# Optimization experiments

Hardware: AMD Instinct MI355X
Metric: run time of the kernel (lower is better)

The kernel has to match this reference:

```python
import jax, jax.numpy as jnp
import numpy as np

N, E, F, H, L = 10000, 200000, 28, 256, 6
NUM_ATOM, NUM_BOND = 100, 24

def ssp(x):
    # shifted softplus used by SchNet
    return jax.nn.softplus(x) - jnp.log(2.0)

def setup_inputs() -> dict:
    key = jax.random.key(0)
    ks = iter(jax.random.split(key, 64))
    def nrm(shape, scale=0.05):
        return jax.random.normal(next(ks), shape, dtype=jnp.float32) * scale
    inp = {}
    inp['atom_type'] = jax.random.randint(next(ks), (N,), 0, NUM_ATOM)
    inp['r_feat'] = jax.random.normal(next(ks), (N, F), dtype=jnp.float32)
    inp['p_feat'] = jax.random.normal(next(ks), (N, F), dtype=jnp.float32)
    inp['pos'] = jax.random.normal(next(ks), (N, 3), dtype=jnp.float32) * 3.0
    inp['edge_index'] = jax.random.randint(next(ks), (2, E), 0, N)
    inp['edge_type_r'] = jax.random.randint(next(ks), (E,), 0, NUM_BOND)
    inp['edge_type_p'] = jax.random.randint(next(ks), (E,), 0, NUM_BOND)
    # learned parameters
    inp['atom_emb_table'] = nrm((NUM_ATOM, H // 2), 1.0)
    inp['feat_W'] = nrm((F, H // 2))                       # atom_feat_embedding (no bias)
    inp['bond_emb_table'] = nrm((NUM_BOND, H), 1.0)        # edge encoder bond embedding
    inp['edge_mlp_W1'] = nrm((1, H)); inp['edge_mlp_b1'] = jnp.zeros((H,), jnp.float32)
    inp['edge_mlp_W2'] = nrm((H, H)); inp['edge_mlp_b2'] = jnp.zeros((H,), jnp.float32)
    inp['cat_W1'] = nrm((2 * H, H)); inp['cat_b1'] = jnp.zeros((H,), jnp.float32)
    inp['cat_W2'] = nrm((H, H)); inp['cat_b2'] = jnp.zeros((H,), jnp.float32)
    # SchNet interaction blocks, stacked over L layers
    inp['filt_W1'] = nrm((L, H, H)); inp['filt_b1'] = jnp.zeros((L, H), jnp.float32)
    inp['filt_W2'] = nrm((L, H, H)); inp['filt_b2'] = jnp.zeros((L, H), jnp.float32)
    inp['lin1_W'] = nrm((L, H, H))
    inp['lin2_W'] = nrm((L, H, H)); inp['lin2_b'] = jnp.zeros((L, H), jnp.float32)
    inp['lin3_W'] = nrm((L, H, H)); inp['lin3_b'] = jnp.zeros((L, H), jnp.float32)
    # grad_global_dist_mlp: 2H -> H -> H/2 -> 1
    inp['grad_W1'] = nrm((2 * H, H)); inp['grad_b1'] = jnp.zeros((H,), jnp.float32)
    inp['grad_W2'] = nrm((H, H // 2)); inp['grad_b2'] = jnp.zeros((H // 2,), jnp.float32)
    inp['grad_W3'] = nrm((H // 2, 1)); inp['grad_b3'] = jnp.zeros((1,), jnp.float32)
    return inp

def _forward(r_feat, p_feat, pos, atom_emb_table, feat_W, bond_emb_table,
             edge_mlp_W1, edge_mlp_b1, edge_mlp_W2, edge_mlp_b2,
             cat_W1, cat_b1, cat_W2, cat_b2,
             filt_W1, filt_b1, filt_W2, filt_b2,
             lin1_W, lin2_W, lin2_b, lin3_W, lin3_b,
             grad_W1, grad_b1, grad_W2, grad_b2, grad_W3, grad_b3,
             atom_type, edge_index, edge_type_r, edge_type_p):
    src, dst = edge_index[0], edge_index[1]
    # node embedding: z = [atom_emb + feat(r), feat(p) - feat(r)]
    ar = r_feat @ feat_W
    ap = p_feat @ feat_W
    z = jnp.concatenate([atom_emb_table[atom_type] + ar, ap - ar], axis=-1)  # (N, H)
    # edge lengths (E, 1)
    d = pos[src] - pos[dst]
    edge_length = jnp.sqrt(jnp.sum(d * d, axis=-1, keepdims=True) + 1e-12)
    # condensed edge embedding 'bond_w_d': mlp(d) * bond_emb(type), r/p branches, then edge_cat MLP
    d_emb = ssp(edge_length @ edge_mlp_W1 + edge_mlp_b1) @ edge_mlp_W2 + edge_mlp_b2  # (E, H)
    attr_r = d_emb * bond_emb_table[edge_type_r]
    attr_p = d_emb * bond_emb_table[edge_type_p]
    edge_attr = jax.nn.relu(jnp.concatenate([attr_r, attr_p], -1) @ cat_W1 + cat_b1) @ cat_W2 + cat_b2  # (E, H)
    # SchNet encoder: L CFConv interaction blocks with residual
    nn_ = z.shape[0]
    def layer(h, p):
        fW1, fb1, fW2, fb2, l1, l2, l2b, l3, l3b = p
        Wf = ssp(edge_attr @ fW1 + fb1) @ fW2 + fb2            # (E, H) continuous filters
        msg = (h @ l1)[src] * Wf                               # gather + modulate
        agg = jax.ops.segment_sum(msg, dst, num_segments=nn_)  # scatter-add to nodes
        return h + (ssp(agg @ l2 + l2b) @ l3 + l3b), None
    node_attr, _ = jax.lax.scan(layer, z, (filt_W1, filt_b1, filt_W2, filt_b2, lin1_W, lin2_W, lin2_b, lin3_W, lin3_b))
    # assemble_atom_pair_feature: [h_row * h_col, edge_attr] -> (E, 2H)
    h_pair = jnp.concatenate([node_attr[src] * node_attr[dst], edge_attr], axis=-1)
    h = jax.nn.relu(h_pair @ grad_W1 + grad_b1)
    h = jax.nn.relu(h @ grad_W2 + grad_b2)
    edge_inv = h @ grad_W3 + grad_b3                           # (E, 1)
    return edge_inv, edge_length

def reference(atom_type, r_feat, p_feat, pos, edge_index, edge_type_r, edge_type_p,
              atom_emb_table, feat_W, bond_emb_table,
              edge_mlp_W1, edge_mlp_b1, edge_mlp_W2, edge_mlp_b2,
              cat_W1, cat_b1, cat_W2, cat_b2,
              filt_W1, filt_b1, filt_W2, filt_b2,
              lin1_W, lin2_W, lin2_b, lin3_W, lin3_b,
              grad_W1, grad_b1, grad_W2, grad_b2, grad_W3, grad_b3):
    return _forward(r_feat, p_feat, pos, atom_emb_table, feat_W, bond_emb_table,
                    edge_mlp_W1, edge_mlp_b1, edge_mlp_W2, edge_mlp_b2,
                    cat_W1, cat_b1, cat_W2, cat_b2,
                    filt_W1, filt_b1, filt_W2, filt_b2,
                    lin1_W, lin2_W, lin2_b, lin3_W, lin3_b,
                    grad_W1, grad_b1, grad_W2, grad_b2, grad_W3, grad_b3,
                    atom_type, edge_index, edge_type_r, edge_type_p)
```

## Files before the change

### kernel.cpp

```cpp
#include <hip/hip_runtime.h>
#include <hip/hip_bf16.h>
#include <math.h>

#define HDIM 256

typedef unsigned short u16;
typedef short short8 __attribute__((ext_vector_type(8)));
typedef _Float16 f16x8 __attribute__((ext_vector_type(8)));
typedef float f32x4 __attribute__((ext_vector_type(4)));

__device__ __forceinline__ float sspf(float x) {
  const float LOG2E = 1.4426950408889634f, LN2 = 0.6931471805599453f;
  float t = exp2f(-fabsf(x) * LOG2E);
  return fmaxf(x, 0.f) + (log2f(1.f + t) - 1.f) * LN2;
}
__device__ __forceinline__ float bf2f(u16 u) {
  union { unsigned int i; float f; } x; x.i = ((unsigned int)u) << 16; return x.f;
}
__device__ __forceinline__ u16 f2bf(float f) {
  union { float f; unsigned int i; } x; x.f = f;
  unsigned int r = x.i + 0x7FFFu + ((x.i >> 16) & 1u);
  return (u16)(r >> 16);
}
__device__ __forceinline__ u16 f2h_bits(float f) {
  _Float16 h = (_Float16)f;
  return __builtin_bit_cast(unsigned short, h);
}
__device__ __forceinline__ float4 ld4f(const float* p) { return *(const float4*)p; }

__device__ __forceinline__ int iw_idx(int row, int col) {
  return row * 256 + ((((col >> 3) ^ (row & 7)) << 3) | (col & 7));
}
__device__ __forceinline__ int ir_idx(int row, int cchunk) {
  return row * 256 + ((cchunk ^ (row & 7)) << 3);
}

template<int DT>
__device__ __forceinline__ f32x4 mma(short8 a, short8 b, f32x4 c) {
  if constexpr (DT == 0)
    return __builtin_amdgcn_mfma_f32_16x16x32_bf16(a, b, c, 0, 0, 0);
  else
    return __builtin_amdgcn_mfma_f32_16x16x32_f16(__builtin_bit_cast(f16x8, a),
                                                  __builtin_bit_cast(f16x8, b), c, 0, 0, 0);
}

__device__ __forceinline__ void zacc(f32x4 (&acc)[4][4]) {
#pragma unroll
  for (int i = 0; i < 4; ++i)
#pragma unroll
    for (int j = 0; j < 4; ++j) { acc[i][j][0]=0.f; acc[i][j][1]=0.f; acc[i][j][2]=0.f; acc[i][j][3]=0.f; }
}

template<int NSTEPS, int BT_N, int NTW, int DT, bool WRAP8, typename ATR>
__device__ __forceinline__ void gemm44(f32x4 (&acc)[4][4], const u16* __restrict__ bt,
                                       const u16* __restrict__ inter,
                                       int w, int m, int quad, ATR atr) {
#pragma unroll
  for (int ks = 0; ks < NSTEPS; ++ks) {
    short8 bf[NTW];
#pragma unroll
    for (int nt = 0; nt < NTW; ++nt)
      bf[nt] = *(const short8*)(bt + (size_t)ks * (BT_N * 32)
                                + (w * (NTW * 16) + nt * 16 + m) * 32 + quad * 8);
    int kchunk = (WRAP8 ? (ks & 7) : ks) * 4 + quad;
#pragma unroll
    for (int mt = 0; mt < 4; ++mt) {
      short8 af = *(const short8*)&inter[ir_idx(mt * 16 + m, kchunk)];
      af = atr(mt, ks, af);
#pragma unroll
      for (int nt = 0; nt < NTW; ++nt)
        acc[mt][nt] = mma<DT>(af, bf[nt], acc[mt][nt]);
    }
  }
}

template<int NTW, int ACT, int OF>
__device__ __forceinline__ void store_inter44(u16* inter, int w, int m, int quad,
                                              const f32x4 (&acc)[4][4], const float* bias) {
#pragma unroll
  for (int mt = 0; mt < 4; ++mt)
#pragma unroll
    for (int nt = 0; nt < NTW; ++nt) {
      int col = w * (NTW * 16) + nt * 16 + m;
      float bv = bias[col];
#pragma unroll
      for (int r = 0; r < 4; ++r) {
        int row = mt * 16 + quad * 4 + r;
        float x = acc[mt][nt][r] + bv;
        if (ACT == 1) x = fmaxf(x, 0.f);
        else if (ACT == 2) x = sspf(x);
        inter[iw_idx(row, col)] = (OF == 0) ? f2bf(x) : f2h_bits(x);
      }
    }
}

template<int NTW, int ACT>
__device__ __forceinline__ void store_edge44(u16* C, int row0, int w, int m, int quad,
                                             const f32x4 (&acc)[4][4], const float* bias) {
#pragma unroll
  for (int mt = 0; mt < 4; ++mt)
#pragma unroll
    for (int nt = 0; nt < NTW; ++nt) {
      int col = w * (NTW * 16) + nt * 16 + m;
      float bv = bias[col];
#pragma unroll
      for (int r = 0; r < 4; ++r) {
        float x = acc[mt][nt][r] + bv;
        if (ACT == 1) x = fmaxf(x, 0.f);
        C[(size_t)(row0 + mt * 16 + quad * 4 + r) * HDIM + col] = f2bf(x);
      }
    }
}

template<int NTW, int ACT, int CM>
__device__ __forceinline__ void store_node44(float* C, int row0, int w, int m, int quad,
                                             const f32x4 (&acc)[4][4], const float* bias, int M) {
#pragma unroll
  for (int mt = 0; mt < 4; ++mt)
#pragma unroll
    for (int nt = 0; nt < NTW; ++nt) {
      int col = w * (NTW * 16) + nt * 16 + m;
      float bv = bias ? bias[col] : 0.f;
#pragma unroll
      for (int r = 0; r < 4; ++r) {
        int row = row0 + mt * 16 + quad * 4 + r;
        if (row < M) {
          float x = acc[mt][nt][r] + bv;
          if (ACT == 2) x = sspf(x);
          size_t idx = (size_t)row * HDIM + col;
          if (CM == 1) x += C[idx];
          C[idx] = x;
        }
      }
    }
}

struct EncArgs {
  const int* se_e; const float* lenp; const float* W1; const float* b1;
  const u16* btA; const float* bA;
  const float* bondT; const int* etr; const int* etp;
  const u16* btB; const float* bB;
  const u16* btC; const float* bC;
  u16* outp;
};
__global__ __launch_bounds__(256, 3) void encoder_k(EncArgs a) {
  __shared__ u16 inter[64 * 256];
  __shared__ u16 bondL[24 * 264];
  const int t = threadIdx.x;
  const int w = t >> 6, lane = t & 63, m = lane & 15, quad = lane >> 4;
  const int row0 = blockIdx.x * 64;
  auto idt = [](int, int, short8 v) { return v; };

  for (int i = t; i < 24 * 256; i += 256) {
    int r = i >> 8, c = i & 255;
    bondL[r * 264 + c] = f2h_bits(a.bondT[r * 256 + c]);
  }
  int brv[4], bpv[4];
#pragma unroll
  for (int mt = 0; mt < 4; ++mt) {
    int eo = a.se_e[row0 + mt * 16 + m];
    brv[mt] = a.etr[eo]; bpv[mt] = a.etp[eo];
  }
  {
    int row = t >> 2;
    float len = a.lenp[a.se_e[row0 + row]];
#pragma unroll
    for (int c = 0; c < 8; ++c) {
      int chunk = (t & 3) + c * 4, k = chunk * 8;
      float4 w0 = ld4f(a.W1 + k), w1 = ld4f(a.W1 + k + 4);
      float4 c0 = ld4f(a.b1 + k), c1 = ld4f(a.b1 + k + 4);
      short8 v;
      v[0] = (short)f2bf(sspf(len * w0.x + c0.x)); v[1] = (short)f2bf(sspf(len * w0.y + c0.y));
      v[2] = (short)f2bf(sspf(len * w0.z + c0.z)); v[3] = (short)f2bf(sspf(len * w0.w + c0.w));
      v[4] = (short)f2bf(sspf(len * w1.x + c1.x)); v[5] = (short)f2bf(sspf(len * w1.y + c1.y));
      v[6] = (short)f2bf(sspf(len * w1.z + c1.z)); v[7] = (short)f2bf(sspf(len * w1.w + c1.w));
      *(short8*)&inter[row * 256 + ((chunk ^ (row & 7)) << 3)] = v;
    }
  }
  __syncthreads();
  f32x4 acc[4][4];
  zacc(acc);
  gemm44<8, 256, 4, 0, false>(acc, a.btA, inter, w, m, quad, idt);
  __syncthreads();
  store_inter44<4, 0, 1>(inter, w, m, quad, acc, a.bA);
  __syncthreads();
  zacc(acc);
  auto atrB = [&](int mt, int ks, short8 v) -> short8 {
    int k2 = (ks & 7) * 32 + quad * 8;
    int et = (ks < 8) ? brv[mt] : bpv[mt];
    f16x8 dv = __builtin_bit_cast(f16x8, v);
    f16x8 bd = __builtin_bit_cast(f16x8, *(const short8*)&bondL[et * 264 + k2]);
    return __builtin_bit_cast(short8, dv * bd);
  };
  gemm44<16, 256, 4, 1, true>(acc, a.btB, inter, w, m, quad, atrB);
  __syncthreads();
  store_inter44<4, 1, 0>(inter, w, m, quad, acc, a.bB);
  __syncthreads();
  zacc(acc);
  gemm44<8, 256, 4, 0, false>(acc, a.btC, inter, w, m, quad, idt);
  store_edge44<4, 0>(a.outp, row0, w, m, quad, acc, a.bC);
}

struct FiltArgs { const u16* inA; const u16* bt1; const float* b1; const u16* bt2; const float* b2; u16* outp; };
__global__ __launch_bounds__(256, 3) void filt_k(FiltArgs a) {
  __shared__ u16 inter[64 * 256];
  const int t = threadIdx.x;
  const int w = t >> 6, lane = t & 63, m = lane & 15, quad = lane >> 4;
  const int row0 = blockIdx.x * 64;
  auto idt = [](int, int, short8 v) { return v; };
  {
    int row = t >> 2;
#pragma unroll
    for (int c = 0; c < 8; ++c) {
      int chunk = (t & 3) + c * 4;
      short8 v = *(const short8*)(a.inA + (size_t)(row0 + row) * HDIM + chunk * 8);
      *(short8*)&inter[row * 256 + ((chunk ^ (row & 7)) << 3)] = v;
    }
  }
  __syncthreads();
  f32x4 acc[4][4];
  zacc(acc);
  gemm44<8, 256, 4, 0, false>(acc, a.bt1, inter, w, m, quad, idt);
  __syncthreads();
  store_inter44<4, 2, 0>(inter, w, m, quad, acc, a.b1);
  __syncthreads();
  zacc(acc);
  gemm44<8, 256, 4, 0, false>(acc, a.bt2, inter, w, m, quad, idt);
  store_edge44<4, 0>(a.outp, row0, w, m, quad, acc, a.b2);
}

struct GradArgs {
  const float* h; const int* se_src; const int* se_dst; const int* se_e;
  const u16* eA; const u16* bt1; const float* b1; const u16* bt2; const float* b2;
  const float* W3; const float* b3; float* outp;
};
__global__ __launch_bounds__(256, 3) void gradf_k(GradArgs a) {
  __shared__ u16 inter[64 * 256];
  const int t = threadIdx.x;
  const int w = t >> 6, lane = t & 63, m = lane & 15, quad = lane >> 4;
  const int row0 = blockIdx.x * 64;
  auto idt = [](int, int, short8 v) { return v; };
  {
    int row = t >> 2;
    int s = a.se_src[row0 + row], d = a.se_dst[row0 + row];
#pragma unroll
    for (int c = 0; c < 8; ++c) {
      int chunk = (t & 3) + c * 4, k = chunk * 8;
      const float* xp = a.h + (size_t)s * HDIM + k;
      const float* yp = a.h + (size_t)d * HDIM + k;
      float4 x0 = ld4f(xp), x1 = ld4f(xp + 4);
      float4 y0 = ld4f(yp), y1 = ld4f(yp + 4);
      short8 v;
      v[0] = (short)f2bf(x0.x * y0.x); v[1] = (short)f2bf(x0.y * y0.y);
      v[2] = (short)f2bf(x0.z * y0.z); v[3] = (short)f2bf(x0.w * y0.w);
      v[4] = (short)f2bf(x1.x * y1.x); v[5] = (short)f2bf(x1.y * y1.y);
      v[6] = (short)f2bf(x1.z * y1.z); v[7] = (short)f2bf(x1.w * y1.w);
      *(short8*)&inter[row * 256 + ((chunk ^ (row & 7)) << 3)] = v;
    }
  }
  __syncthreads();
  f32x4 acc[4][4];
  zacc(acc);
  gemm44<8, 256, 4, 0, false>(acc, a.bt1, inter, w, m, quad, idt);
  __syncthreads();
  {
    int row = t >> 2;
#pragma unroll
    for (int c = 0; c < 8; ++c) {
      int chunk = (t & 3) + c * 4;
      short8 v = *(const short8*)(a.eA + (size_t)(row0 + row) * HDIM + chunk * 8);
      *(short8*)&inter[row * 256 + ((chunk ^ (row & 7)) << 3)] = v;
    }
  }
  __syncthreads();
  gemm44<8, 256, 4, 0, false>(acc, a.bt1 + 8 * 256 * 32, inter, w, m, quad, idt);
  __syncthreads();
  store_inter44<4, 1, 0>(inter, w, m, quad, acc, a.b1);
  __syncthreads();
  zacc(acc);
  gemm44<8, 128, 2, 0, false>(acc, a.bt2, inter, w, m, quad, idt);
  float p[4][4];
#pragma unroll
  for (int mt = 0; mt < 4; ++mt) { p[mt][0]=0.f; p[mt][1]=0.f; p[mt][2]=0.f; p[mt][3]=0.f; }
#pragma unroll
  for (int mt = 0; mt < 4; ++mt)
#pragma unroll
    for (int nt = 0; nt < 2; ++nt) {
      int col = w * 32 + nt * 16 + m;
      float w3 = a.W3[col], bv = a.b2[col];
#pragma unroll
      for (int r = 0; r < 4; ++r) p[mt][r] += fmaxf(acc[mt][nt][r] + bv, 0.f) * w3;
    }
  __syncthreads();
  float* red = (float*)inter;
#pragma unroll
  for (int mt = 0; mt < 4; ++mt)
#pragma unroll
    for (int r = 0; r < 4; ++r)
      red[(mt * 16 + quad * 4 + r) * 68 + w * 16 + m] = p[mt][r];
  __syncthreads();
  if (t < 64) {
    float s = a.b3[0];
#pragma unroll
    for (int i = 0; i < 64; ++i) s += red[t * 68 + i];
    a.outp[a.se_e[row0 + t]] = s;
  }
}

struct LinArgs { const float* A; const u16* bt; float* C; int M; };
__global__ __launch_bounds__(256, 3) void lin1_k(LinArgs a) {
  __shared__ u16 inter[64 * 256];
  const int t = threadIdx.x;
  const int w = t >> 6, lane = t & 63, m = lane & 15, quad = lane >> 4;
  const int row0 = blockIdx.x * 64;
  auto idt = [](int, int, short8 v) { return v; };
  {
    int row = t >> 2, grow = row0 + row;
#pragma unroll
    for (int c = 0; c < 8; ++c) {
      int chunk = (t & 3) + c * 4, k = chunk * 8;
      short8 v;
      if (grow < a.M) {
        const float* p = a.A + (size_t)grow * HDIM + k;
        float4 x0 = ld4f(p), x1 = ld4f(p + 4);
        v[0]=(short)f2bf(x0.x); v[1]=(short)f2bf(x0.y); v[2]=(short)f2bf(x0.z); v[3]=(short)f2bf(x0.w);
        v[4]=(short)f2bf(x1.x); v[5]=(short)f2bf(x1.y); v[6]=(short)f2bf(x1.z); v[7]=(short)f2bf(x1.w);
      } else { v = short8{0,0,0,0,0,0,0,0}; }
      *(short8*)&inter[row * 256 + ((chunk ^ (row & 7)) << 3)] = v;
    }
  }
  __syncthreads();
  f32x4 acc[4][4];
  zacc(acc);
  gemm44<8, 256, 4, 0, false>(acc, a.bt, inter, w, m, quad, idt);
  store_node44<4, 0, 0>(a.C, row0, w, m, quad, acc, nullptr, a.M);
}

struct Lin23Args { const float* A; const u16* bt2; const float* b2; const u16* bt3; const float* b3; float* C; int M; };
__global__ __launch_bounds__(256, 3) void lin23_k(Lin23Args a) {
  __shared__ u16 inter[64 * 256];
  const int t = threadIdx.x;
  const int w = t >> 6, lane = t & 63, m = lane & 15, quad = lane >> 4;
  const int row0 = blockIdx.x * 64;
  auto idt = [](int, int, short8 v) { return v; };
  {
    int row = t >> 2, grow = row0 + row;
#pragma unroll
    for (int c = 0; c < 8; ++c) {
      int chunk = (t & 3) + c * 4, k = chunk * 8;
      short8 v;
      if (grow < a.M) {
        const float* p = a.A + (size_t)grow * HDIM + k;
        float4 x0 = ld4f(p), x1 = ld4f(p + 4);
        v[0]=(short)f2bf(x0.x); v[1]=(short)f2bf(x0.y); v[2]=(short)f2bf(x0.z); v[3]=(short)f2bf(x0.w);
        v[4]=(short)f2bf(x1.x); v[5]=(short)f2bf(x1.y); v[6]=(short)f2bf(x1.z); v[7]=(short)f2bf(x1.w);
      } else { v = short8{0,0,0,0,0,0,0,0}; }
      *(short8*)&inter[row * 256 + ((chunk ^ (row & 7)) << 3)] = v;
    }
  }
  __syncthreads();
  f32x4 acc[4][4];
  zacc(acc);
  gemm44<8, 256, 4, 0, false>(acc, a.bt2, inter, w, m, quad, idt);
  __syncthreads();
  store_inter44<4, 2, 0>(inter, w, m, quad, acc, a.b2);
  __syncthreads();
  zacc(acc);
  gemm44<8, 256, 4, 0, false>(acc, a.bt3, inter, w, m, quad, idt);
  store_node44<4, 0, 1>(a.C, row0, w, m, quad, acc, a.b3, a.M);
}

struct WTDesc { const float* src; u16* dst; int K; int Nshift; int fmt; };
struct WTList { WTDesc d[35]; };
__global__ __launch_bounds__(256) void wtrans_k(WTList wl) {
  WTDesc e = wl.d[blockIdx.y];
  int total = e.K << e.Nshift;
  int idx = blockIdx.x * 256 + threadIdx.x;
  if (idx >= total) return;
  int k = idx >> e.Nshift;
  int n = idx & ((1 << e.Nshift) - 1);
  float v = e.src[idx];
  e.dst[((size_t)(k >> 5) << (e.Nshift + 5)) + n * 32 + (k & 31)] = e.fmt ? f2h_bits(v) : f2bf(v);
}

__global__ void node_embed_k(const int* atom_type, const float* r_feat, const float* p_feat,
                             const float* emb, const float* fW, float* z, int N, int F) {
  int n = blockIdx.x;
  int j = threadIdx.x;
  __shared__ float rr[32], pp[32];
  if (j < F) { rr[j] = r_feat[(size_t)n * F + j]; pp[j] = p_feat[(size_t)n * F + j]; }
  __syncthreads();
  float ar = 0.f, ap = 0.f;
  for (int f = 0; f < F; ++f) {
    float wv = fW[f * 128 + j];
    ar += rr[f] * wv;
    ap += pp[f] * wv;
  }
  int at = atom_type[n];
  z[(size_t)n * HDIM + j] = emb[at * 128 + j] + ar;
  z[(size_t)n * HDIM + 128 + j] = ap - ar;
}

__global__ void edge_geom_k(const float* pos, const int* src, const int* dst, float* len_out, int E) {
  int e = blockIdx.x * blockDim.x + threadIdx.x;
  if (e >= E) return;
  int s = src[e], d = dst[e];
  float dx = pos[s * 3 + 0] - pos[d * 3 + 0];
  float dy = pos[s * 3 + 1] - pos[d * 3 + 1];
  float dz = pos[s * 3 + 2] - pos[d * 3 + 2];
  len_out[e] = sqrtf(dx * dx + dy * dy + dz * dz + 1e-12f);
}

__global__ void zero_k(float4* p, int n4) {
  int i = blockIdx.x * 256 + threadIdx.x;
  if (i < n4) p[i] = make_float4(0.f, 0.f, 0.f, 0.f);
}
__global__ void zero_int_k(int* p, int n) {
  int i = blockIdx.x * 256 + threadIdx.x;
  if (i < n) p[i] = 0;
}
__global__ void hist_k(const int* dst, int* cnt, int E) {
  int e = blockIdx.x * 256 + threadIdx.x;
  if (e < E) atomicAdd(&cnt[dst[e]], 1);
}
__global__ __launch_bounds__(256) void scan_k(const int* cnt, int* rowstart, int N) {
  __shared__ int part[256];
  int t = threadIdx.x;
  int chunk = (N + 255) / 256;
  int lo = t * chunk, hi = lo + chunk; if (hi > N) hi = N; if (lo > N) lo = N;
  int s = 0;
  for (int i = lo; i < hi; ++i) s += cnt[i];
  part[t] = s;
  __syncthreads();
  for (int off = 1; off < 256; off <<= 1) {
    int v = (t >= off) ? part[t - off] : 0;
    __syncthreads();
    part[t] += v;
    __syncthreads();
  }
  int run = (t == 0) ? 0 : part[t - 1];
  for (int i = lo; i < hi; ++i) { rowstart[i] = run; run += cnt[i]; }
  if (t == 255) rowstart[N] = run;
}
__global__ void fill_k(const int* src, const int* dst, const int* rowstart, int* cursor,
                       int* se_src, int* se_dst, int* se_e, int E) {
  int e = blockIdx.x * 256 + threadIdx.x;
  if (e >= E) return;
  int d = dst[e];
  int p = atomicAdd(&cursor[d], 1);
  int idx = rowstart[d] + p;
  se_src[idx] = src[e];
  se_dst[idx] = d;
  se_e[idx] = e;
}

__global__ __launch_bounds__(256) void gather_k(const float* hh, const u16* Wf,
                                                const int* se_src, const int* rowstart,
                                                float* agg, int N) {
  int n = blockIdx.x;
  int j = threadIdx.x;
  int s0 = rowstart[n], s1 = rowstart[n + 1];
  float acc = 0.f;
  for (int i = s0; i < s1; ++i)
    acc += hh[(size_t)se_src[i] * HDIM + j] * bf2f(Wf[(size_t)i * HDIM + j]);
  agg[(size_t)n * HDIM + j] = acc;
}

extern "C" void kernel_launch(void* const* d_in, const int* in_sizes, int n_in,
                              void* d_out, int out_size, void* d_ws, size_t ws_size,
                              hipStream_t stream) {
  const int* atom_type = (const int*)d_in[0];
  const float* r_feat  = (const float*)d_in[1];
  const float* p_feat  = (const float*)d_in[2];
  const float* pos     = (const float*)d_in[3];
  const int* eidx      = (const int*)d_in[4];
  const int* etype_r   = (const int*)d_in[5];
  const int* etype_p   = (const int*)d_in[6];
  const float* atom_emb = (const float*)d_in[7];
  const float* feat_W   = (const float*)d_in[8];
  const float* bondT    = (const float*)d_in[9];
  const float* e_W1     = (const float*)d_in[10];
  const float* e_b1     = (const float*)d_in[11];
  const float* e_W2     = (const float*)d_in[12];
  const float* e_b2     = (const float*)d_in[13];
  const float* cat_W1   = (const float*)d_in[14];
  const float* cat_b1   = (const float*)d_in[15];
  const float* cat_W2   = (const float*)d_in[16];
  const float* cat_b2   = (const float*)d_in[17];
  const float* filt_W1  = (const float*)d_in[18];
  const float* filt_b1  = (const float*)d_in[19];
  const float* filt_W2  = (const float*)d_in[20];
  const float* filt_b2  = (const float*)d_in[21];
  const float* lin1_W   = (const float*)d_in[22];
  const float* lin2_W   = (const float*)d_in[23];
  const float* lin2_b   = (const float*)d_in[24];
  const float* lin3_W   = (const float*)d_in[25];
  const float* lin3_b   = (const float*)d_in[26];
  const float* grad_W1  = (const float*)d_in[27];
  const float* grad_b1  = (const float*)d_in[28];
  const float* grad_W2  = (const float*)d_in[29];
  const float* grad_b2  = (const float*)d_in[30];
  const float* grad_W3  = (const float*)d_in[31];
  const float* grad_b3  = (const float*)d_in[32];

  const int N = in_sizes[0];
  const int F = in_sizes[1] / N;
  const int E = in_sizes[4] / 2;
  const int L = in_sizes[18] / (HDIM * HDIM);
  const int* srcI = eidx;
  const int* dstI = eidx + E;
  float* out = (float*)d_out;

  const size_t BT_ELEMS = (size_t)(32 * 65536 + 2 * 131072 + 32768);
  size_t need = 2 * (size_t)E * HDIM * 2 + 3 * (size_t)N * HDIM * 4 + BT_ELEMS * 2
              + (size_t)(3 * E + 3 * N + 1) * 4 + 64;
  if (ws_size < need) {
    int n4 = (out_size + 3) / 4;
    zero_k<<<(n4 + 255) / 256, 256, 0, stream>>>((float4*)d_out, n4);
    return;
  }
  char* base = (char*)d_ws;
  u16* eA = (u16*)base; base += (size_t)E * HDIM * 2;
  u16* Wf = (u16*)base; base += (size_t)E * HDIM * 2;
  float* h   = (float*)base; base += (size_t)N * HDIM * 4;
  float* hh  = (float*)base; base += (size_t)N * HDIM * 4;
  float* agg = (float*)base; base += (size_t)N * HDIM * 4;
  u16* bt = (u16*)base; base += BT_ELEMS * 2;
  int* se_src = (int*)base; base += (size_t)E * 4;
  int* se_dst = (int*)base; base += (size_t)E * 4;
  int* se_e   = (int*)base; base += (size_t)E * 4;
  int* cnt    = (int*)base; base += (size_t)N * 4;
  int* cursor = (int*)base; base += (size_t)N * 4;
  int* rowstart = (int*)base; base += ((size_t)N + 1) * 4;

  size_t off = 0;
  u16* bt_eW2  = bt + off; off += 65536;
  u16* bt_cat1 = bt + off; off += 131072;
  u16* bt_cat2 = bt + off; off += 65536;
  u16* bt_f1[6]; u16* bt_f2[6]; u16* bt_l1[6]; u16* bt_l2[6]; u16* bt_l3[6];
  for (int l = 0; l < 6; ++l) { bt_f1[l] = bt + off; off += 65536; }
  for (int l = 0; l < 6; ++l) { bt_f2[l] = bt + off; off += 65536; }
  for (int l = 0; l < 6; ++l) { bt_l1[l] = bt + off; off += 65536; }
  for (int l = 0; l < 6; ++l) { bt_l2[l] = bt + off; off += 65536; }
  for (int l = 0; l < 6; ++l) { bt_l3[l] = bt + off; off += 65536; }
  u16* bt_g1 = bt + off; off += 131072;
  u16* bt_g2 = bt + off; off += 32768;

  WTList wl;
  int wi = 0;
  wl.d[wi++] = WTDesc{e_W2, bt_eW2, 256, 8, 0};
  wl.d[wi++] = WTDesc{cat_W1, bt_cat1, 512, 8, 1};
  wl.d[wi++] = WTDesc{cat_W2, bt_cat2, 256, 8, 0};
  for (int l = 0; l < 6; ++l) wl.d[wi++] = WTDesc{filt_W1 + (size_t)l * 65536, bt_f1[l], 256, 8, 0};
  for (int l = 0; l < 6; ++l) wl.d[wi++] = WTDesc{filt_W2 + (size_t)l * 65536, bt_f2[l], 256, 8, 0};
  for (int l = 0; l < 6; ++l) wl.d[wi++] = WTDesc{lin1_W + (size_t)l * 65536, bt_l1[l], 256, 8, 0};
  for (int l = 0; l < 6; ++l) wl.d[wi++] = WTDesc{lin2_W + (size_t)l * 65536, bt_l2[l], 256, 8, 0};
  for (int l = 0; l < 6; ++l) wl.d[wi++] = WTDesc{lin3_W + (size_t)l * 65536, bt_l3[l], 256, 8, 0};
  wl.d[wi++] = WTDesc{grad_W1, bt_g1, 512, 8, 0};
  wl.d[wi++] = WTDesc{grad_W2, bt_g2, 256, 7, 0};
  wtrans_k<<<dim3(512, 35), 256, 0, stream>>>(wl);

  const int EB = E / 64;
  const int NBK = (N + 63) / 64;
  const int EBLK = (E + 255) / 256;

  zero_int_k<<<(2 * N + 255) / 256, 256, 0, stream>>>(cnt, 2 * N);
  hist_k<<<EBLK, 256, 0, stream>>>(dstI, cnt, E);
  scan_k<<<1, 256, 0, stream>>>(cnt, rowstart, N);
  fill_k<<<EBLK, 256, 0, stream>>>(srcI, dstI, rowstart, cursor, se_src, se_dst, se_e, E);

  node_embed_k<<<N, 128, 0, stream>>>(atom_type, r_feat, p_feat, atom_emb, feat_W, h, N, F);
  edge_geom_k<<<EBLK, 256, 0, stream>>>(pos, srcI, dstI, out + E, E);

  EncArgs ea;
  ea.se_e = se_e; ea.lenp = out + E; ea.W1 = e_W1; ea.b1 = e_b1;
  ea.btA = bt_eW2; ea.bA = e_b2;
  ea.bondT = bondT; ea.etr = etype_r; ea.etp = etype_p;
  ea.btB = bt_cat1; ea.bB = cat_b1;
  ea.btC = bt_cat2; ea.bC = cat_b2;
  ea.outp = eA;
  encoder_k<<<EB, 256, 0, stream>>>(ea);

  for (int l = 0; l < L; ++l) {
    const size_t bo = (size_t)l * HDIM;
    FiltArgs fa{eA, bt_f1[l], filt_b1 + bo, bt_f2[l], filt_b2 + bo, Wf};
    filt_k<<<EB, 256, 0, stream>>>(fa);
    LinArgs la{h, bt_l1[l], hh, N};
    lin1_k<<<NBK, 256, 0, stream>>>(la);
    gather_k<<<N, 256, 0, stream>>>(hh, Wf, se_src, rowstart, agg, N);
    Lin23Args l23{agg, bt_l2[l], lin2_b + bo, bt_l3[l], lin3_b + bo, h, N};
    lin23_k<<<NBK, 256, 0, stream>>>(l23);
  }

  GradArgs ga;
  ga.h = h; ga.se_src = se_src; ga.se_dst = se_dst; ga.se_e = se_e;
  ga.eA = eA; ga.bt1 = bt_g1; ga.b1 = grad_b1; ga.bt2 = bt_g2; ga.b2 = grad_b2;
  ga.W3 = grad_W3; ga.b3 = grad_b3; ga.outp = out;
  gradf_k<<<EB, 256, 0, stream>>>(ga);
}
```

Measured before the change: 1.686 ms.

## Fuse filter MLP with neighbor gather via segmented atomic accumulation

Each layer's filter MLP kernel now keeps the bf16 filter output in shared memory and immediately multiplies it by gathered hh[src] rows. It then accumulates runs of equal destination node within the 64-edge tile and flushes each run to agg with float atomics, replacing the separate Wf buffer and per-node gather kernel. This removes a 200000x256 bf16 write and read per layer. It adds a zeroing pass for agg, atomic contention at tile boundaries and nondeterministic summation order. The encoder output store is also staged through padded shared memory for coalesced vector writes.

```diff
diff --git a/kernel.cpp b/kernel.cpp
--- a/kernel.cpp
+++ b/kernel.cpp
@@ -3,6 +3,7 @@
 #include <math.h>
 
 #define HDIM 256
+#define PSTR 264
 
 typedef unsigned short u16;
 typedef short short8 __attribute__((ext_vector_type(8)));
@@ -95,8 +96,8 @@
 }
 
 template<int NTW, int ACT>
-__device__ __forceinline__ void store_edge44(u16* C, int row0, int w, int m, int quad,
-                                             const f32x4 (&acc)[4][4], const float* bias) {
+__device__ __forceinline__ void store_plain44(u16* inter, int w, int m, int quad,
+                                              const f32x4 (&acc)[4][4], const float* bias) {
 #pragma unroll
   for (int mt = 0; mt < 4; ++mt)
 #pragma unroll
@@ -107,9 +108,18 @@
       for (int r = 0; r < 4; ++r) {
         float x = acc[mt][nt][r] + bv;
         if (ACT == 1) x = fmaxf(x, 0.f);
-        C[(size_t)(row0 + mt * 16 + quad * 4 + r) * HDIM + col] = f2bf(x);
+        inter[(mt * 16 + quad * 4 + r) * PSTR + col] = f2bf(x);
       }
     }
+}
+
+__device__ __forceinline__ void copy_out(u16* C, int row0, const u16* inter, int t) {
+#pragma unroll
+  for (int c = 0; c < 8; ++c) {
+    int idx = c * 256 + t;
+    int row = idx >> 5, c8 = idx & 31;
+    *(short8*)(C + (size_t)(row0 + row) * HDIM + c8 * 8) = *(const short8*)&inter[row * PSTR + c8 * 8];
+  }
 }
 
 template<int NTW, int ACT, int CM>
@@ -144,7 +154,7 @@
   u16* outp;
 };
 __global__ __launch_bounds__(256, 3) void encoder_k(EncArgs a) {
-  __shared__ u16 inter[64 * 256];
+  __shared__ u16 inter[64 * PSTR];
   __shared__ u16 bondL[24 * 264];
   const int t = threadIdx.x;
   const int w = t >> 6, lane = t & 63, m = lane & 15, quad = lane >> 4;
@@ -198,22 +208,30 @@
   __syncthreads();
   zacc(acc);
   gemm44<8, 256, 4, 0, false>(acc, a.btC, inter, w, m, quad, idt);
-  store_edge44<4, 0>(a.outp, row0, w, m, quad, acc, a.bC);
-}
-
-struct FiltArgs { const u16* inA; const u16* bt1; const float* b1; const u16* bt2; const float* b2; u16* outp; };
-__global__ __launch_bounds__(256, 3) void filt_k(FiltArgs a) {
-  __shared__ u16 inter[64 * 256];
+  __syncthreads();
+  store_plain44<4, 0>(inter, w, m, quad, acc, a.bC);
+  __syncthreads();
+  copy_out(a.outp, row0, inter, t);
+}
+
+struct FGArgs {
+  const u16* eA; const u16* bt1; const float* b1; const u16* bt2; const float* b2;
+  const float* hh; const int* se_src; const int* se_dst; float* agg;
+};
+__global__ __launch_bounds__(256, 3) void fgat_k(FGArgs a) {
+  __shared__ u16 inter[64 * PSTR];
+  __shared__ int sl[64], dl[64];
   const int t = threadIdx.x;
   const int w = t >> 6, lane = t & 63, m = lane & 15, quad = lane >> 4;
   const int row0 = blockIdx.x * 64;
   auto idt = [](int, int, short8 v) { return v; };
+  if (t < 64) { sl[t] = a.se_src[row0 + t]; dl[t] = a.se_dst[row0 + t]; }
   {
     int row = t >> 2;
 #pragma unroll
     for (int c = 0; c < 8; ++c) {
       int chunk = (t & 3) + c * 4;
-      short8 v = *(const short8*)(a.inA + (size_t)(row0 + row) * HDIM + chunk * 8);
+      short8 v = *(const short8*)(a.eA + (size_t)(row0 + row) * HDIM + chunk * 8);
       *(short8*)&inter[row * 256 + ((chunk ^ (row & 7)) << 3)] = v;
     }
   }
@@ -226,7 +244,20 @@
   __syncthreads();
   zacc(acc);
   gemm44<8, 256, 4, 0, false>(acc, a.bt2, inter, w, m, quad, idt);
-  store_edge44<4, 0>(a.outp, row0, w, m, quad, acc, a.b2);
+  __syncthreads();
+  store_plain44<4, 0>(inter, w, m, quad, acc, a.b2);
+  __syncthreads();
+  float accv = 0.f;
+  int cur = dl[0];
+  for (int i = 0; i < 64; ++i) {
+    int dn = dl[i];
+    if (dn != cur) {
+      atomicAdd(&a.agg[(size_t)cur * HDIM + t], accv);
+      accv = 0.f; cur = dn;
+    }
+    accv += a.hh[(size_t)sl[i] * HDIM + t] * bf2f(inter[i * PSTR + t]);
+  }
+  atomicAdd(&a.agg[(size_t)cur * HDIM + t], accv);
 }
 
 struct GradArgs {
@@ -452,18 +483,6 @@
   se_src[idx] = src[e];
   se_dst[idx] = d;
   se_e[idx] = e;
-}
-
-__global__ __launch_bounds__(256) void gather_k(const float* hh, const u16* Wf,
-                                                const int* se_src, const int* rowstart,
-                                                float* agg, int N) {
-  int n = blockIdx.x;
-  int j = threadIdx.x;
-  int s0 = rowstart[n], s1 = rowstart[n + 1];
-  float acc = 0.f;
-  for (int i = s0; i < s1; ++i)
-    acc += hh[(size_t)se_src[i] * HDIM + j] * bf2f(Wf[(size_t)i * HDIM + j]);
-  agg[(size_t)n * HDIM + j] = acc;
 }
 
 extern "C" void kernel_launch(void* const* d_in, const int* in_sizes, int n_in,
@@ -512,7 +531,7 @@
   float* out = (float*)d_out;
 
   const size_t BT_ELEMS = (size_t)(32 * 65536 + 2 * 131072 + 32768);
-  size_t need = 2 * (size_t)E * HDIM * 2 + 3 * (size_t)N * HDIM * 4 + BT_ELEMS * 2
+  size_t need = (size_t)E * HDIM * 2 + 3 * (size_t)N * HDIM * 4 + BT_ELEMS * 2
               + (size_t)(3 * E + 3 * N + 1) * 4 + 64;
   if (ws_size < need) {
     int n4 = (out_size + 3) / 4;
@@ -521,7 +540,6 @@
   }
   char* base = (char*)d_ws;
   u16* eA = (u16*)base; base += (size_t)E * HDIM * 2;
-  u16* Wf = (u16*)base; base += (size_t)E * HDIM * 2;
   float* h   = (float*)base; base += (size_t)N * HDIM * 4;
   float* hh  = (float*)base; base += (size_t)N * HDIM * 4;
   float* agg = (float*)base; base += (size_t)N * HDIM * 4;
@@ -563,6 +581,7 @@
   const int EB = E / 64;
   const int NBK = (N + 63) / 64;
   const int EBLK = (E + 255) / 256;
+  const int NZ4 = N * HDIM / 4;
 
   zero_int_k<<<(2 * N + 255) / 256, 256, 0, stream>>>(cnt, 2 * N);
   hist_k<<<EBLK, 256, 0, stream>>>(dstI, cnt, E);
@@ -583,11 +602,11 @@
 
   for (int l = 0; l < L; ++l) {
     const size_t bo = (size_t)l * HDIM;
-    FiltArgs fa{eA, bt_f1[l], filt_b1 + bo, bt_f2[l], filt_b2 + bo, Wf};
-    filt_k<<<EB, 256, 0, stream>>>(fa);
     LinArgs la{h, bt_l1[l], hh, N};
     lin1_k<<<NBK, 256, 0, stream>>>(la);
-    gather_k<<<N, 256, 0, stream>>>(hh, Wf, se_src, rowstart, agg, N);
+    zero_k<<<(NZ4 + 255) / 256, 256, 0, stream>>>((float4*)agg, NZ4);
+    FGArgs fg{eA, bt_f1[l], filt_b1 + bo, bt_f2[l], filt_b2 + bo, hh, se_src, se_dst, agg};
+    fgat_k<<<EB, 256, 0, stream>>>(fg);
     Lin23Args l23{agg, bt_l2[l], lin2_b + bo, bt_l3[l], lin3_b + bo, h, N};
     lin23_k<<<NBK, 256, 0, stream>>>(l23);
   }
```

After: 1.921 ms. +13.9%, slower.
